# Kernel optimization log

Hardware: AMD Instinct MI355X
Metric: run time of the kernel (lower is better)

## Reference

```python
import jax, jax.numpy as jnp
import numpy as np

N_NODES = 50000
N_EDGES = 800000
D = 128  # in_dim == hidden_dim
N_CLASSES = 2


def setup_inputs() -> dict:
    key = jax.random.key(0)
    ks = jax.random.split(key, 8)
    x = jax.random.normal(ks[0], (N_NODES, D), dtype=jnp.float32)
    edge_index = jax.random.randint(ks[1], (2, N_EDGES), 0, N_NODES)
    s = 1.0 / np.sqrt(D)
    W1 = jax.random.normal(ks[2], (D, D), dtype=jnp.float32) * s
    b1 = jnp.zeros((D,), jnp.float32)
    W2 = jax.random.normal(ks[3], (D, D), dtype=jnp.float32) * s
    b2 = jnp.zeros((D,), jnp.float32)
    Wc = jax.random.normal(ks[4], (D, N_CLASSES), dtype=jnp.float32) * s
    bc = jnp.zeros((N_CLASSES,), jnp.float32)
    return {"x": x, "edge_index": edge_index, "W1": W1, "b1": b1,
            "W2": W2, "b2": b2, "Wc": Wc, "bc": bc}


def gcn_layer(x, W, b, src, dst, n):
    """PyG GCNConv: h = D^{-1/2}(A+I)D^{-1/2} (x @ W) + b, self-loops added."""
    h = x @ W  # [n, d_out]
    loop = jnp.arange(n)
    src2 = jnp.concatenate([src, loop])  # [E+n]
    dst2 = jnp.concatenate([dst, loop])
    deg = jax.ops.segment_sum(jnp.ones_like(dst2, dtype=h.dtype), dst2, num_segments=n)
    inv_sqrt = jax.lax.rsqrt(deg)  # deg >= 1 thanks to self-loops
    coef = inv_sqrt[src2] * inv_sqrt[dst2]  # [E+n]
    msg = h[src2] * coef[:, None]  # gather + scale
    out = jax.ops.segment_sum(msg, dst2, num_segments=n)  # scatter-add
    return out + b


def reference(x, edge_index, W1, b1, W2, b2, Wc, bc):
    src, dst = edge_index[0], edge_index[1]
    n = x.shape[0]
    h = jax.nn.relu(gcn_layer(x, W1, b1, src, dst, n))
    h = jax.nn.relu(gcn_layer(h, W2, b2, src, dst, n))
    g = h.mean(axis=0)  # mean pool over nodes -> [hidden]
    logits = g @ Wc + bc  # [2]
    return jax.nn.log_softmax(logits, axis=0)
```

## Files before the change

### kernel.cpp

```cpp
#include <hip/hip_runtime.h>

#define D 128
#define PAD 64
#define SCAP 12288
typedef unsigned char  u8;
typedef unsigned short u16;
typedef unsigned int   u32;
typedef unsigned long long u64;
typedef __attribute__((ext_vector_type(8))) short bf16x8;
typedef __attribute__((ext_vector_type(4))) float f32x4;
typedef __attribute__((ext_vector_type(2))) float f32x2;


__device__ __forceinline__ float b2f_lo(u32 w) {
    u32 x = w << 16; float f; __builtin_memcpy(&f, &x, 4); return f;
}
__device__ __forceinline__ float b2f_hi(u32 w) {
    u32 x = w & 0xffff0000u; float f; __builtin_memcpy(&f, &x, 4); return f;
}
__device__ __forceinline__ u16 f2b(float f) {
    u32 x; __builtin_memcpy(&x, &f, 4);
    u32 lsb = (x >> 16) & 1u;
    x += 0x7fffu + lsb;
    return (u16)(x >> 16);
}
__device__ __forceinline__ u8 f2fp8(float f) {
    int p = __builtin_amdgcn_cvt_pk_fp8_f32(f, f, 0, false);
    return (u8)(p & 0xff);
}
__device__ __forceinline__ f32x2 fp8lo(u32 w) {
    return __builtin_amdgcn_cvt_pk_f32_fp8((int)w, false);
}
__device__ __forceinline__ f32x2 fp8hi(u32 w) {
    return __builtin_amdgcn_cvt_pk_f32_fp8((int)w, true);
}

__global__ void k_init(float* __restrict__ gpool,
                       const void* p0, const void* p1, const void* p2, const void* p3,
                       const void* p4, const void* p5, const void* p6,
                       int* __restrict__ flags, u16* __restrict__ WT1,
                       u16* __restrict__ WTf2,
                       const int* __restrict__ src, const int* __restrict__ dst, int E,
                       u32* __restrict__ slist, int* __restrict__ slcur, int pb) {
    __shared__ u16 t[128 * 130];
    __shared__ int s_wbf;
    __shared__ u32 lcnt[128], lbase[128];
    const int bid = blockIdx.x, tid = threadIdx.x;
    if (bid == 0) {
        uint4* g4 = (uint4*)gpool;
        #pragma unroll
        for (int k = 0; k < 8; ++k) g4[tid + k * 256] = (uint4){0, 0, 0, 0};
        const void* ps[7] = {p0, p1, p2, p3, p4, p5, p6};
        const int   nw[7] = {64, 64, 64, 64, 64, 64, 1};
        int wave = tid >> 6, lane = tid & 63;
        for (int b = wave; b < 7; b += 4) {
            u32 w = (lane < nw[b]) ? ((const u32*)ps[b])[lane] : 0u;
            int nzb = (w != 0u);
            u32 e = (w >> 7) & 0xFFu;
            int hitb = nzb && (e > 100u && e < 140u);
            u64 nzm = __ballot(nzb);
            u64 hm  = __ballot(hitb);
            int nz = __popcll(nzm), hits = __popcll(hm);
            if (lane == 0) flags[b] = (nz == 0) || (2 * hits >= nz);
        }
        return;
    }
    if (bid >= 3) {
        const int pid = bid - 3;
        const int E4 = E >> 2;
        const int i4 = pid * 256 + tid;
        if (tid < 128) lcnt[tid] = 0;
        __syncthreads();
        u32 wpk[4]; int gg[4]; u32 loc[4];
        const int valid = i4 < E4;
        if (valid) {
            int4 dd = ((const int4*)dst)[i4];
            int4 sv = ((const int4*)src)[i4];
            int d[4] = {dd.x, dd.y, dd.z, dd.w};
            int s[4] = {sv.x, sv.y, sv.z, sv.w};
            #pragma unroll
            for (int k = 0; k < 4; ++k) {
                gg[k]  = d[k] >> 9;
                wpk[k] = ((u32)d[k] << 16) | (u32)(s[k] & 0xffff);
                loc[k] = atomicAdd(&lcnt[gg[k]], 1u);
            }
        }
        __syncthreads();
        if (tid < 128) {
            u32 c = lcnt[tid];
            lbase[tid] = c ? atomicAdd((u32*)&slcur[tid], c) : 0u;
        }
        __syncthreads();
        if (valid) {
            #pragma unroll
            for (int k = 0; k < 4; ++k) {
                u32 p = lbase[gg[k]] + loc[k];
                if (p < SCAP) slist[(size_t)gg[k] * SCAP + p] = wpk[k];
            }
        }
        if (pid == pb - 1 && tid < (E & 3)) {
            int e = (E & ~3) + tid;
            int d = dst[e], s = src[e];
            u32 p = atomicAdd((u32*)&slcur[d >> 9], 1u);
            if (p < SCAP) slist[(size_t)(d >> 9) * SCAP + p] = ((u32)d << 16) | (u32)(s & 0xffff);
        }
        return;
    }
    const void* Wp = (bid == 1) ? p1 : p3;
    if (tid < 64) {
        u32 w = ((const u32*)Wp)[tid];
        int nzb = (w != 0u);
        u32 e = (w >> 7) & 0xFFu;
        int hitb = nzb && (e > 100u && e < 140u);
        u64 nzm = __ballot(nzb);
        u64 hm  = __ballot(hitb);
        if (tid == 0) {
            int nz = __popcll(nzm), hits = __popcll(hm);
            s_wbf = (nz == 0) || (2 * hits >= nz);
        }
    }
    __syncthreads();
    if (s_wbf) {
        const u32* W2w = (const u32*)Wp;
        for (int i = tid; i < 8192; i += 256) {
            u32 w = W2w[i];
            int k = i >> 6, n2 = (i & 63) * 2;
            t[k * 130 + n2]     = (u16)(w & 0xffffu);
            t[k * 130 + n2 + 1] = (u16)(w >> 16);
        }
    } else {
        const float* Wf = (const float*)Wp;
        for (int i = tid; i < 16384; i += 256) {
            int k = i >> 7, nn = i & 127;
            t[k * 130 + nn] = f2b(Wf[i]);
        }
    }
    __syncthreads();
    if (bid == 1) {
        for (int i = tid; i < 16384; i += 256) {
            int nn = i >> 7, kk = i & 127;
            WT1[i] = t[kk * 130 + nn];
        }
    } else {
        for (int fi = tid; fi < 16384; fi += 256) {
            int j = fi & 7, lane = (fi >> 3) & 63, tc = fi >> 9;
            int tt = tc >> 3, c = tc & 7, m = lane & 15, quad = lane >> 4;
            int k = tt * 32 + quad * 8 + j, col = c * 16 + m;
            WTf2[fi] = t[k * 130 + col];
        }
    }
}

__device__ __forceinline__ void gemm_body16(int bid, const void* __restrict__ Ap, int abf,
                                            const u16* __restrict__ WT,
                                            u8* __restrict__ C, int n, u8* cst) {
    const int wave = threadIdx.x >> 6, lane = threadIdx.x & 63;
    const int m = lane & 15, quad = lane >> 4;
    const int r0 = bid * 64 + wave * 16;
    int arow = r0 + m; if (arow > n - 1) arow = n - 1;

    bf16x8 afr[4];
    if (abf) {
        const u16* Ab = (const u16*)Ap + (size_t)arow * D + quad * 8;
        #pragma unroll
        for (int t = 0; t < 4; ++t) afr[t] = *(const bf16x8*)(Ab + t * 32);
    } else {
        const float* Af = (const float*)Ap + (size_t)arow * D + quad * 8;
        #pragma unroll
        for (int t = 0; t < 4; ++t) {
            float4 f0 = *(const float4*)(Af + t * 32);
            float4 f1 = *(const float4*)(Af + t * 32 + 4);
            bf16x8 a;
            a[0] = (short)f2b(f0.x); a[1] = (short)f2b(f0.y);
            a[2] = (short)f2b(f0.z); a[3] = (short)f2b(f0.w);
            a[4] = (short)f2b(f1.x); a[5] = (short)f2b(f1.y);
            a[6] = (short)f2b(f1.z); a[7] = (short)f2b(f1.w);
            afr[t] = a;
        }
    }
    f32x4 acc[8];
    #pragma unroll
    for (int c = 0; c < 8; ++c) acc[c] = (f32x4){0.f, 0.f, 0.f, 0.f};
    const u16* wb = WT + (size_t)m * D + quad * 8;
    #pragma unroll
    for (int t = 0; t < 4; ++t) {
        #pragma unroll
        for (int c = 0; c < 8; ++c) {
            bf16x8 b = *(const bf16x8*)(wb + (size_t)c * 16 * D + t * 32);
            acc[c] = __builtin_amdgcn_mfma_f32_16x16x32_bf16(afr[t], b, acc[c], 0, 0, 0);
        }
    }
    u8* myrows = cst + wave * 16 * 132;
    #pragma unroll
    for (int c = 0; c < 8; ++c) {
        #pragma unroll
        for (int r = 0; r < 4; ++r)
            myrows[(quad * 4 + r) * 132 + c * 16 + m] = f2fp8(acc[c][r]);
    }
    int r = lane >> 2, off = (lane & 3) * 32;
    int grow = r0 + r;
    if (grow < n) {
        uint4 v0 = *(const uint4*)(myrows + r * 132 + off);
        uint4 v1 = *(const uint4*)(myrows + r * 132 + off + 16);
        *(uint4*)(C + (size_t)grow * D + off)      = v0;
        *(uint4*)(C + (size_t)grow * D + off + 16) = v1;
    }
}

__global__ __launch_bounds__(256) void k_fused(
        const void* __restrict__ Ap, const u16* __restrict__ WT,
        const int* __restrict__ flags, u8* __restrict__ C, int n, int gb, int fb0,
        int nsl, const u32* __restrict__ slist, const int* __restrict__ slcur,
        int* __restrict__ cnt, u16* __restrict__ csrp) {
    __shared__ __align__(16) u8 cst[4 * 16 * 132];
    __shared__ int lc[512];
    if (blockIdx.x < (u32)gb) {
        __shared__ int s_abf;
        if (threadIdx.x == 0) s_abf = flags[0];
        __syncthreads();
        gemm_body16(blockIdx.x, Ap, s_abf, WT, C, n, cst);
        return;
    }
    if (blockIdx.x < (u32)fb0) return;
    const int s = blockIdx.x - fb0;
    if (s >= nsl) return;
    const int base = s << 9;
    const int tid = threadIdx.x;
    lc[tid] = 0; lc[tid + 256] = 0;
    __syncthreads();
    int len = slcur[s]; if (len > SCAP) len = SCAP;
    const u32* sl = slist + (size_t)s * SCAP;
    for (int e = tid; e < len; e += 256) {
        u32 w = sl[e];
        int d = (int)(w >> 16);
        int pos = atomicAdd(&lc[d - base], 1);
        if (pos < PAD) csrp[(size_t)d * PAD + pos] = (u16)(w & 0xffffu);
    }
    __syncthreads();
    #pragma unroll
    for (int i = tid; i < 512; i += 256) {
        int node = base + i;
        if (node < n) cnt[node] = lc[i];
    }
}

__global__ __launch_bounds__(256) void k_scale(u8* __restrict__ h,
                                               const int* __restrict__ cnt, int n) {
    int i = blockIdx.x * 256 + threadIdx.x;
    int row = i >> 5;
    if (row >= n) return;
    float invd = rsqrtf(1.0f + (float)cnt[row]);
    u32* p = (u32*)h + i;
    u32 w = *p;
    f32x2 lo = fp8lo(w), hi = fp8hi(w);
    int pk = __builtin_amdgcn_cvt_pk_fp8_f32(lo[0] * invd, lo[1] * invd, 0, false);
    pk = __builtin_amdgcn_cvt_pk_fp8_f32(hi[0] * invd, hi[1] * invd, pk, true);
    *p = (u32)pk;
}

__device__ __forceinline__ f32x4 agg_row4(int node, int lane, float invd, int mcnt,
                                          const u8* __restrict__ H,
                                          const u16* __restrict__ csrp,
                                          const void* __restrict__ bias, int bbf) {
    const int q = lane & 31, half = lane >> 5;
    int idx = csrp[(size_t)node * PAD + lane];
    f32x4 acc = (f32x4){0.f, 0.f, 0.f, 0.f};
    const int NP = (mcnt + 1) >> 1;
    int p = 0;
    for (; p + 8 <= NP; p += 8) {
        u32 w[8]; int ok[8];
        #pragma unroll
        for (int k = 0; k < 8; ++k) {
            int e = 2 * (p + k) + half;
            int s = __shfl(idx, e);
            w[k] = *(const u32*)(H + (size_t)s * D + q * 4);
            ok[k] = e < mcnt;
        }
        #pragma unroll
        for (int k = 0; k < 8; ++k) {
            if (ok[k]) {
                f32x2 lo = fp8lo(w[k]), hi = fp8hi(w[k]);
                acc[0] += lo[0]; acc[1] += lo[1]; acc[2] += hi[0]; acc[3] += hi[1];
            }
        }
    }
    for (; p < NP; ++p) {
        int e = 2 * p + half;
        int s = __shfl(idx, e);
        u32 w = *(const u32*)(H + (size_t)s * D + q * 4);
        if (e < mcnt) {
            f32x2 lo = fp8lo(w), hi = fp8hi(w);
            acc[0] += lo[0]; acc[1] += lo[1]; acc[2] += hi[0]; acc[3] += hi[1];
        }
    }
    acc[0] += __shfl_xor(acc[0], 32);
    acc[1] += __shfl_xor(acc[1], 32);
    acc[2] += __shfl_xor(acc[2], 32);
    acc[3] += __shfl_xor(acc[3], 32);
    {
        u32 w = *(const u32*)(H + (size_t)node * D + q * 4);
        f32x2 lo = fp8lo(w), hi = fp8hi(w);
        acc[0] += lo[0]; acc[1] += lo[1]; acc[2] += hi[0]; acc[3] += hi[1];
    }
    float b0, b1, b2, b3;
    if (bbf) {
        u32 w0 = ((const u32*)bias)[2 * q], w1 = ((const u32*)bias)[2 * q + 1];
        b0 = b2f_lo(w0); b1 = b2f_hi(w0); b2 = b2f_lo(w1); b3 = b2f_hi(w1);
    } else {
        float4 b = ((const float4*)bias)[q];
        b0 = b.x; b1 = b.y; b2 = b.z; b3 = b.w;
    }
    f32x4 o;
    o[0] = fmaxf(fmaf(invd, acc[0], b0), 0.f);
    o[1] = fmaxf(fmaf(invd, acc[1], b1), 0.f);
    o[2] = fmaxf(fmaf(invd, acc[2], b2), 0.f);
    o[3] = fmaxf(fmaf(invd, acc[3], b3), 0.f);
    return o;
}

__global__ __launch_bounds__(256) void k_aggemm(
        const u8* __restrict__ h, const int* __restrict__ cnt,
        const u16* __restrict__ csrp, const void* __restrict__ bias,
        const int* __restrict__ flags, int fidx,
        const u16* __restrict__ WTf, u8* __restrict__ C, int n) {
    __shared__ int s_bbf;
    __shared__ __align__(16) float accA[16][132];
    __shared__ float sinv[16];
    if (threadIdx.x == 0) s_bbf = flags[fidx];
    __syncthreads();
    const int wv = threadIdx.x >> 6, lane = threadIdx.x & 63;
    const int base = blockIdx.x * 16;
    #pragma unroll
    for (int i = 0; i < 4; ++i) {
        int m = wv + i * 4;
        int node = base + m;
        f32x4 o = (f32x4){0.f, 0.f, 0.f, 0.f};
        float invd = 0.f;
        if (node < n) {
            int cn = cnt[node];
            invd = rsqrtf(1.0f + (float)cn);
            int mcnt = cn < PAD ? cn : PAD;
            o = agg_row4(node, lane, invd, mcnt, h, csrp, bias, s_bbf);
        }
        if (lane < 32) {
            float4 v = {o[0], o[1], o[2], o[3]};
            *(float4*)&accA[m][4 * lane] = v;
        }
        if (lane == 0) sinv[m] = invd;
    }
    __syncthreads();
    const int m0 = lane & 15, quad = lane >> 4;
    f32x4 acc[2];
    acc[0] = (f32x4){0.f, 0.f, 0.f, 0.f};
    acc[1] = (f32x4){0.f, 0.f, 0.f, 0.f};
    #pragma unroll
    for (int t = 0; t < 4; ++t) {
        const float* ap = &accA[m0][t * 32 + quad * 8];
        float4 f0 = *(const float4*)ap;
        float4 f1 = *(const float4*)(ap + 4);
        bf16x8 a;
        a[0] = (short)f2b(f0.x); a[1] = (short)f2b(f0.y);
        a[2] = (short)f2b(f0.z); a[3] = (short)f2b(f0.w);
        a[4] = (short)f2b(f1.x); a[5] = (short)f2b(f1.y);
        a[6] = (short)f2b(f1.z); a[7] = (short)f2b(f1.w);
        #pragma unroll
        for (int cc = 0; cc < 2; ++cc) {
            int c = wv * 2 + cc;
            bf16x8 b = *(const bf16x8*)(WTf + ((size_t)(t * 8 + c) * 64 + lane) * 8);
            acc[cc] = __builtin_amdgcn_mfma_f32_16x16x32_bf16(a, b, acc[cc], 0, 0, 0);
        }
    }
    #pragma unroll
    for (int cc = 0; cc < 2; ++cc) {
        int c = wv * 2 + cc;
        #pragma unroll
        for (int r = 0; r < 4; ++r) {
            int row = base + quad * 4 + r;
            if (row < n)
                C[(size_t)row * D + c * 16 + m0] = f2fp8(sinv[quad * 4 + r] * acc[cc][r]);
        }
    }
}

__global__ __launch_bounds__(256) void k_agg2p(const u8* __restrict__ h,
                                               const int* __restrict__ cnt,
                                               const u16* __restrict__ csrp,
                                               const void* __restrict__ bias,
                                               const int* __restrict__ flags, int fidx,
                                               float* __restrict__ gpool, int n) {
    __shared__ int s_bbf;
    __shared__ float sacc[4][128];
    if (threadIdx.x == 0) s_bbf = flags[fidx];
    __syncthreads();
    int wv   = threadIdx.x >> 6;
    int lane = threadIdx.x & 63;
    int node = blockIdx.x * 4 + wv;
    f32x4 o = (f32x4){0.f, 0.f, 0.f, 0.f};
    if (node < n) {
        int cn = cnt[node];
        float invd = rsqrtf(1.0f + (float)cn);
        int mcnt = cn < PAD ? cn : PAD;
        o = agg_row4(node, lane, invd, mcnt, h, csrp, bias, s_bbf);
    }
    if (lane < 32) {
        float4 v = {o[0], o[1], o[2], o[3]};
        *(float4*)&sacc[wv][4 * lane] = v;
    }
    __syncthreads();
    if (wv == 0) {
        float a = sacc[0][lane] + sacc[1][lane] + sacc[2][lane] + sacc[3][lane];
        float b = sacc[0][lane + 64] + sacc[1][lane + 64] + sacc[2][lane + 64] + sacc[3][lane + 64];
        float* rep = gpool + (size_t)(blockIdx.x & 63) * 128;
        atomicAdd(&rep[lane],      a);
        atomicAdd(&rep[lane + 64], b);
    }
}

__global__ void k_final(const float* __restrict__ gpool, const void* __restrict__ Wc,
                        const void* __restrict__ bc, const int* __restrict__ flags,
                        void* __restrict__ outp, int n) {
    __shared__ float s0[128], s1[128];
    int t = threadIdx.x;
    float acc = 0.f;
    #pragma unroll 8
    for (int r = 0; r < 64; ++r) acc += gpool[r * 128 + t];
    float g = acc / (float)n;
    float w0, w1;
    if (flags[5]) { u32 w = ((const u32*)Wc)[t]; w0 = b2f_lo(w); w1 = b2f_hi(w); }
    else          { float2 w = ((const float2*)Wc)[t]; w0 = w.x; w1 = w.y; }
    s0[t] = g * w0;
    s1[t] = g * w1;
    __syncthreads();
    if (t == 0) {
        float l0, l1;
        if (flags[6]) { u32 b = ((const u32*)bc)[0]; l0 = b2f_lo(b); l1 = b2f_hi(b); }
        else          { const float* b = (const float*)bc; l0 = b[0]; l1 = b[1]; }
        for (int i = 0; i < 128; ++i) { l0 += s0[i]; l1 += s1[i]; }
        float m = fmaxf(l0, l1);
        float lse = m + logf(expf(l0 - m) + expf(l1 - m));
        if (flags[0]) {
            u16* o = (u16*)outp;
            o[0] = f2b(l0 - lse);
            o[1] = f2b(l1 - lse);
        } else {
            float* o = (float*)outp;
            o[0] = l0 - lse;
            o[1] = l1 - lse;
        }
    }
}

extern "C" void kernel_launch(void* const* d_in, const int* in_sizes, int n_in,
                              void* d_out, int out_size, void* d_ws, size_t ws_size,
                              hipStream_t stream) {
    const void* x  = d_in[0];
    const int*  ei = (const int*)d_in[1];
    const void* W1 = d_in[2];
    const void* b1 = d_in[3];
    const void* W2 = d_in[4];
    const void* b2 = d_in[5];
    const void* Wc = d_in[6];
    const void* bc = d_in[7];

    const int n = in_sizes[0] / D;
    const int E = in_sizes[1] / 2;

    char* wsp = (char*)d_ws;
    size_t off = 0;
    auto carve = [&](size_t bytes) -> void* {
        void* p = wsp + off;
        off = (off + bytes + 255) & ~(size_t)255;
        return p;
    };
    const int nsl = (n + 511) >> 9;
    u8*    h0    = (u8*)carve((size_t)n * D);
    u8*    h1    = (u8*)carve((size_t)n * D);
    int*   cnt   = (int*)carve((size_t)n * 4);
    u16*   csrp  = (u16*)carve((size_t)n * PAD * 2);
    u32*   slist = (u32*)carve((size_t)nsl * SCAP * 4);
    int*   slcur = (int*)carve(128 * 4);
    float* gpool = (float*)carve(64 * 128 * 4);
    int*   flags = (int*)carve(16 * 4);
    u16*   WT1   = (u16*)carve((size_t)D * D * 2);
    u16*   WTf2  = (u16*)carve((size_t)D * D * 2);
    (void)ws_size; (void)n_in; (void)out_size;

    const int* srcI = ei;
    const int* dstI = ei + E;

    const int pb  = ((E >> 2) + 255) / 256;
    const int gb  = (n + 63) / 64;
    const int fb0 = (gb + 7) & ~7;
    const int sb  = (n * 32 + 255) / 256;
    const int gb3 = (n + 15) / 16;
    const int ab  = (n + 3) / 4;

    hipMemsetAsync(slcur, 0, 128 * 4, stream);
    k_init  <<<3 + pb, 256, 0, stream>>>(gpool, x, W1, b1, W2, b2, Wc, bc, flags,
                                         WT1, WTf2, srcI, dstI, E, slist, slcur, pb);
    k_fused <<<fb0 + nsl, 256, 0, stream>>>(x, WT1, flags, h0, n,
                                            gb, fb0, nsl, slist, slcur, cnt, csrp);
    k_scale <<<sb, 256, 0, stream>>>(h0, cnt, n);
    k_aggemm<<<gb3, 256, 0, stream>>>(h0, cnt, csrp, b1, flags, 2, WTf2, h1, n);
    k_agg2p <<<ab, 256, 0, stream>>>(h1, cnt, csrp, b2, flags, 4, gpool, n);
    k_final <<<1, 128, 0, stream>>>(gpool, Wc, bc, flags, d_out, n);
}
```

Measured before the change: 201.3 us.

## Stage W1 fragments in LDS and process 128 rows per GEMM block

```diff
diff --git a/kernel.cpp b/kernel.cpp
--- a/kernel.cpp
+++ b/kernel.cpp
@@ -38,7 +38,7 @@
 __global__ void k_init(float* __restrict__ gpool,
                        const void* p0, const void* p1, const void* p2, const void* p3,
                        const void* p4, const void* p5, const void* p6,
-                       int* __restrict__ flags, u16* __restrict__ WT1,
+                       int* __restrict__ flags, u16* __restrict__ WTf1,
                        u16* __restrict__ WTf2,
                        const int* __restrict__ src, const int* __restrict__ dst, int E,
                        u32* __restrict__ slist, int* __restrict__ slcur, int pb) {
@@ -107,6 +107,7 @@
         return;
     }
     const void* Wp = (bid == 1) ? p1 : p3;
+    u16* WTf      = (bid == 1) ? WTf1 : WTf2;
     if (tid < 64) {
         u32 w = ((const u32*)Wp)[tid];
         int nzb = (w != 0u);
@@ -136,96 +137,112 @@
         }
     }
     __syncthreads();
-    if (bid == 1) {
-        for (int i = tid; i < 16384; i += 256) {
-            int nn = i >> 7, kk = i & 127;
-            WT1[i] = t[kk * 130 + nn];
-        }
-    } else {
-        for (int fi = tid; fi < 16384; fi += 256) {
-            int j = fi & 7, lane = (fi >> 3) & 63, tc = fi >> 9;
-            int tt = tc >> 3, c = tc & 7, m = lane & 15, quad = lane >> 4;
-            int k = tt * 32 + quad * 8 + j, col = c * 16 + m;
-            WTf2[fi] = t[k * 130 + col];
-        }
-    }
-}
-
-__device__ __forceinline__ void gemm_body16(int bid, const void* __restrict__ Ap, int abf,
-                                            const u16* __restrict__ WT,
-                                            u8* __restrict__ C, int n, u8* cst) {
-    const int wave = threadIdx.x >> 6, lane = threadIdx.x & 63;
-    const int m = lane & 15, quad = lane >> 4;
-    const int r0 = bid * 64 + wave * 16;
-    int arow = r0 + m; if (arow > n - 1) arow = n - 1;
-
-    bf16x8 afr[4];
-    if (abf) {
-        const u16* Ab = (const u16*)Ap + (size_t)arow * D + quad * 8;
-        #pragma unroll
-        for (int t = 0; t < 4; ++t) afr[t] = *(const bf16x8*)(Ab + t * 32);
-    } else {
-        const float* Af = (const float*)Ap + (size_t)arow * D + quad * 8;
-        #pragma unroll
-        for (int t = 0; t < 4; ++t) {
-            float4 f0 = *(const float4*)(Af + t * 32);
-            float4 f1 = *(const float4*)(Af + t * 32 + 4);
-            bf16x8 a;
-            a[0] = (short)f2b(f0.x); a[1] = (short)f2b(f0.y);
-            a[2] = (short)f2b(f0.z); a[3] = (short)f2b(f0.w);
-            a[4] = (short)f2b(f1.x); a[5] = (short)f2b(f1.y);
-            a[6] = (short)f2b(f1.z); a[7] = (short)f2b(f1.w);
-            afr[t] = a;
-        }
-    }
-    f32x4 acc[8];
-    #pragma unroll
-    for (int c = 0; c < 8; ++c) acc[c] = (f32x4){0.f, 0.f, 0.f, 0.f};
-    const u16* wb = WT + (size_t)m * D + quad * 8;
-    #pragma unroll
-    for (int t = 0; t < 4; ++t) {
-        #pragma unroll
-        for (int c = 0; c < 8; ++c) {
-            bf16x8 b = *(const bf16x8*)(wb + (size_t)c * 16 * D + t * 32);
-            acc[c] = __builtin_amdgcn_mfma_f32_16x16x32_bf16(afr[t], b, acc[c], 0, 0, 0);
-        }
-    }
-    u8* myrows = cst + wave * 16 * 132;
-    #pragma unroll
-    for (int c = 0; c < 8; ++c) {
-        #pragma unroll
-        for (int r = 0; r < 4; ++r)
-            myrows[(quad * 4 + r) * 132 + c * 16 + m] = f2fp8(acc[c][r]);
-    }
-    int r = lane >> 2, off = (lane & 3) * 32;
-    int grow = r0 + r;
-    if (grow < n) {
-        uint4 v0 = *(const uint4*)(myrows + r * 132 + off);
-        uint4 v1 = *(const uint4*)(myrows + r * 132 + off + 16);
-        *(uint4*)(C + (size_t)grow * D + off)      = v0;
-        *(uint4*)(C + (size_t)grow * D + off + 16) = v1;
+    for (int fi = tid; fi < 16384; fi += 256) {
+        int j = fi & 7, lane = (fi >> 3) & 63, tc = fi >> 9;
+        int tt = tc >> 3, c = tc & 7, m = lane & 15, quad = lane >> 4;
+        int k = tt * 32 + quad * 8 + j, col = c * 16 + m;
+        WTf[fi] = t[k * 130 + col];
     }
 }
 
 __global__ __launch_bounds__(256) void k_fused(
-        const void* __restrict__ Ap, const u16* __restrict__ WT,
-        const int* __restrict__ flags, u8* __restrict__ C, int n, int gb, int fb0,
+        const void* __restrict__ Ap, const u16* __restrict__ WTf1,
+        const int* __restrict__ flags, u8* __restrict__ C, int n, int gb1, int fb0,
         int nsl, const u32* __restrict__ slist, const int* __restrict__ slcur,
         int* __restrict__ cnt, u16* __restrict__ csrp) {
-    __shared__ __align__(16) u8 cst[4 * 16 * 132];
+    __shared__ __align__(16) u8 sbuf[32768];
     __shared__ int lc[512];
-    if (blockIdx.x < (u32)gb) {
+    const int tid = threadIdx.x;
+    if (blockIdx.x < (u32)gb1) {
         __shared__ int s_abf;
-        if (threadIdx.x == 0) s_abf = flags[0];
+        u16* wfrag = (u16*)sbuf;
+        for (int i = tid; i < 2048; i += 256)
+            ((uint4*)wfrag)[i] = ((const uint4*)WTf1)[i];
+        if (tid == 0) s_abf = flags[0];
         __syncthreads();
-        gemm_body16(blockIdx.x, Ap, s_abf, WT, C, n, cst);
+        const int abf = s_abf;
+        const int wv = tid >> 6, lane = tid & 63;
+        const int m = lane & 15, quad = lane >> 4;
+        const int r0 = blockIdx.x * 128 + wv * 32;
+        int ar0 = r0 + m;      if (ar0 > n - 1) ar0 = n - 1;
+        int ar1 = r0 + 16 + m; if (ar1 > n - 1) ar1 = n - 1;
+
+        bf16x8 a0[4], a1[4];
+        if (abf) {
+            const u16* A0 = (const u16*)Ap + (size_t)ar0 * D + quad * 8;
+            const u16* A1 = (const u16*)Ap + (size_t)ar1 * D + quad * 8;
+            #pragma unroll
+            for (int t = 0; t < 4; ++t) {
+                a0[t] = *(const bf16x8*)(A0 + t * 32);
+                a1[t] = *(const bf16x8*)(A1 + t * 32);
+            }
+        } else {
+            const float* A0 = (const float*)Ap + (size_t)ar0 * D + quad * 8;
+            const float* A1 = (const float*)Ap + (size_t)ar1 * D + quad * 8;
+            #pragma unroll
+            for (int t = 0; t < 4; ++t) {
+                float4 f0 = *(const float4*)(A0 + t * 32);
+                float4 f1 = *(const float4*)(A0 + t * 32 + 4);
+                float4 g0 = *(const float4*)(A1 + t * 32);
+                float4 g1 = *(const float4*)(A1 + t * 32 + 4);
+                bf16x8 a, b;
+                a[0] = (short)f2b(f0.x); a[1] = (short)f2b(f0.y);
+                a[2] = (short)f2b(f0.z); a[3] = (short)f2b(f0.w);
+                a[4] = (short)f2b(f1.x); a[5] = (short)f2b(f1.y);
+                a[6] = (short)f2b(f1.z); a[7] = (short)f2b(f1.w);
+                b[0] = (short)f2b(g0.x); b[1] = (short)f2b(g0.y);
+                b[2] = (short)f2b(g0.z); b[3] = (short)f2b(g0.w);
+                b[4] = (short)f2b(g1.x); b[5] = (short)f2b(g1.y);
+                b[6] = (short)f2b(g1.z); b[7] = (short)f2b(g1.w);
+                a0[t] = a; a1[t] = b;
+            }
+        }
+        f32x4 acc0[8], acc1[8];
+        #pragma unroll
+        for (int c = 0; c < 8; ++c) {
+            acc0[c] = (f32x4){0.f, 0.f, 0.f, 0.f};
+            acc1[c] = (f32x4){0.f, 0.f, 0.f, 0.f};
+        }
+        #pragma unroll
+        for (int t = 0; t < 4; ++t) {
+            #pragma unroll
+            for (int c = 0; c < 8; ++c) {
+                bf16x8 b = *(const bf16x8*)(wfrag + ((size_t)(t * 8 + c) * 64 + lane) * 8);
+                acc0[c] = __builtin_amdgcn_mfma_f32_16x16x32_bf16(a0[t], b, acc0[c], 0, 0, 0);
+                acc1[c] = __builtin_amdgcn_mfma_f32_16x16x32_bf16(a1[t], b, acc1[c], 0, 0, 0);
+            }
+        }
+        __syncthreads();
+        #pragma unroll
+        for (int c = 0; c < 8; ++c) {
+            #pragma unroll
+            for (int r = 0; r < 4; ++r) {
+                int lr = wv * 32 + quad * 4 + r;
+                sbuf[lr * 132 + c * 16 + m]        = f2fp8(acc0[c][r]);
+                sbuf[(lr + 16) * 132 + c * 16 + m] = f2fp8(acc1[c][r]);
+            }
+        }
+        __syncthreads();
+        int lr = tid >> 1, off = (tid & 1) * 64;
+        int grow = blockIdx.x * 128 + lr;
+        if (grow < n) {
+            const u8* rp = sbuf + lr * 132 + off;
+            uint4 v0 = *(const uint4*)(rp);
+            uint4 v1 = *(const uint4*)(rp + 16);
+            uint4 v2 = *(const uint4*)(rp + 32);
+            uint4 v3 = *(const uint4*)(rp + 48);
+            u8* gp = C + (size_t)grow * D + off;
+            *(uint4*)(gp)      = v0;
+            *(uint4*)(gp + 16) = v1;
+            *(uint4*)(gp + 32) = v2;
+            *(uint4*)(gp + 48) = v3;
+        }
         return;
     }
     if (blockIdx.x < (u32)fb0) return;
     const int s = blockIdx.x - fb0;
     if (s >= nsl) return;
     const int base = s << 9;
-    const int tid = threadIdx.x;
     lc[tid] = 0; lc[tid + 256] = 0;
     __syncthreads();
     int len = slcur[s]; if (len > SCAP) len = SCAP;
@@ -481,7 +498,7 @@
     int*   slcur = (int*)carve(128 * 4);
     float* gpool = (float*)carve(64 * 128 * 4);
     int*   flags = (int*)carve(16 * 4);
-    u16*   WT1   = (u16*)carve((size_t)D * D * 2);
+    u16*   WTf1  = (u16*)carve((size_t)D * D * 2);
     u16*   WTf2  = (u16*)carve((size_t)D * D * 2);
     (void)ws_size; (void)n_in; (void)out_size;
 
@@ -489,17 +506,17 @@
     const int* dstI = ei + E;
 
     const int pb  = ((E >> 2) + 255) / 256;
-    const int gb  = (n + 63) / 64;
-    const int fb0 = (gb + 7) & ~7;
+    const int gb1 = (n + 127) / 128;
+    const int fb0 = (gb1 + 7) & ~7;
     const int sb  = (n * 32 + 255) / 256;
     const int gb3 = (n + 15) / 16;
     const int ab  = (n + 3) / 4;
 
     hipMemsetAsync(slcur, 0, 128 * 4, stream);
     k_init  <<<3 + pb, 256, 0, stream>>>(gpool, x, W1, b1, W2, b2, Wc, bc, flags,
-                                         WT1, WTf2, srcI, dstI, E, slist, slcur, pb);
-    k_fused <<<fb0 + nsl, 256, 0, stream>>>(x, WT1, flags, h0, n,
-                                            gb, fb0, nsl, slist, slcur, cnt, csrp);
+                                         WTf1, WTf2, srcI, dstI, E, slist, slcur, pb);
+    k_fused <<<fb0 + nsl, 256, 0, stream>>>(x, WTf1, flags, h0, n,
+                                            gb1, fb0, nsl, slist, slcur, cnt, csrp);
     k_scale <<<sb, 256, 0, stream>>>(h0, cnt, n);
     k_aggemm<<<gb3, 256, 0, stream>>>(h0, cnt, csrp, b1, flags, 2, WTf2, h1, n);
     k_agg2p <<<ab, 256, 0, stream>>>(h1, cnt, csrp, b2, flags, 4, gpool, n);
```

Result: faster. 192.6 us (-4.3%).
